# Kernel tuning notes

Measured on AMD Instinct MI355X. Metric: run time of the kernel, lower is better.

Reference implementation:

```python
import jax, jax.numpy as jnp
import numpy as np

N_NODES = 100000
N_EDGES = 1600000
IN_C, HID_C, OUT_C = 128, 64, 40


def setup_inputs() -> dict:
    key = jax.random.key(0)
    ks = jax.random.split(key, 8)
    x = jax.random.normal(ks[0], (N_NODES, IN_C), dtype=jnp.float32)
    edge_index = jax.random.randint(ks[1], (2, N_EDGES), 0, N_NODES, dtype=jnp.int64)
    # Glorot-ish init for weights
    W1 = jax.random.normal(ks[2], (IN_C, HID_C), dtype=jnp.float32) / np.sqrt(IN_C)
    W2 = jax.random.normal(ks[3], (HID_C, HID_C), dtype=jnp.float32) / np.sqrt(HID_C)
    W3 = jax.random.normal(ks[4], (HID_C, OUT_C), dtype=jnp.float32) / np.sqrt(HID_C)
    b1 = jnp.zeros((HID_C,), jnp.float32)
    b2 = jnp.zeros((HID_C,), jnp.float32)
    b3 = jnp.zeros((OUT_C,), jnp.float32)
    return {"x": x, "edge_index": edge_index, "W1": W1, "b1": b1,
            "W2": W2, "b2": b2, "W3": W3, "b3": b3}


def _gcn_prep(edge_index, num_nodes):
    # PyG GCNConv: add self-loops, symmetric normalization with edge_weight=1.
    src = jnp.concatenate([edge_index[0], jnp.arange(num_nodes, dtype=edge_index.dtype)])
    dst = jnp.concatenate([edge_index[1], jnp.arange(num_nodes, dtype=edge_index.dtype)])
    deg = jax.ops.segment_sum(jnp.ones_like(dst, dtype=jnp.float32), dst,
                              num_segments=num_nodes)
    dis = jnp.where(deg > 0, jax.lax.rsqrt(deg), 0.0)  # deg^-1/2, inf->0
    norm = dis[src] * dis[dst]  # per-edge symmetric norm
    return src, dst, norm


def _gcn_conv(x, W, b, src, dst, norm, num_nodes):
    h = x @ W                                # [N, F_out], linear (no bias)
    msg = h[src] * norm[:, None]             # gather + scale, [E_total, F_out]
    out = jax.ops.segment_sum(msg, dst, num_segments=num_nodes)
    return out + b                           # conv bias after aggregation


def reference(x, edge_index, W1, b1, W2, b2, W3, b3):
    n = x.shape[0]
    src, dst, norm = _gcn_prep(edge_index, n)
    h = jax.nn.relu(_gcn_conv(x, W1, b1, src, dst, norm, n))
    h = jax.nn.relu(_gcn_conv(h, W2, b2, src, dst, norm, n))
    h = _gcn_conv(h, W3, b3, src, dst, norm, n)
    return jax.nn.log_softmax(h, axis=1)
```

## Files before the change

### kernel.cpp

```cpp
#include <hip/hip_runtime.h>
#include <cstdint>
#include <cstddef>
#include <math.h>

#define NN 100000
#define NE 1600000
#define NB ((NN + 255) / 256)
#define EB 400
#define EPB (NE / EB)
#define CAP 5120

#define GT_NODES 128
#define GT_KC 32
#define GT_STRIDE 132

typedef unsigned short u16;

__device__ __forceinline__ float bf2f(u16 u) {
    union { unsigned i; float f; } c; c.i = ((unsigned)u) << 16; return c.f;
}
__device__ __forceinline__ u16 f2bf(float f) {
    union { float f; unsigned int i; } c; c.f = f;
    unsigned int lsb = (c.i >> 16) & 1u;
    return (u16)((c.i + 0x7fffu + lsb) >> 16);
}
__device__ __forceinline__ unsigned int pack2(float a, float b) {
    return (unsigned int)f2bf(a) | ((unsigned int)f2bf(b) << 16);
}

__device__ __forceinline__ int load_idx(const void* ei, int isI64, int pos) {
    if (isI64) return (int)((const long long*)ei)[pos];
    return ((const int*)ei)[pos];
}

__global__ __launch_bounds__(256) void k_build(const void* __restrict__ ei,
                                               int* __restrict__ cursor,
                                               int* __restrict__ csr_tmp) {
    __shared__ int sbuf[EPB];
    __shared__ int dbuf[EPB];
    __shared__ int cnt[NB];
    __shared__ int basel[NB];
    __shared__ int anynz;

    const int* p = (const int*)ei;
    if (threadIdx.x == 0) anynz = 0;
    for (int i = threadIdx.x; i < NB; i += 256) cnt[i] = 0;
    __syncthreads();
    int nz = 0;
    for (int i = threadIdx.x; i < 1024; i += 256) nz |= (p[2 * i + 1] != 0);
    if (nz) anynz = 1;
    __syncthreads();
    int isI64 = (anynz == 0);

    int base = blockIdx.x * EPB;
    for (int i = threadIdx.x; i < EPB; i += 256) {
        int s = load_idx(ei, isI64, base + i);
        int d = load_idx(ei, isI64, NE + base + i);
        sbuf[i] = s;
        dbuf[i] = d;
        atomicAdd(&cnt[d >> 8], 1);
    }
    __syncthreads();
    for (int j = threadIdx.x; j < NB; j += 256) {
        int c = cnt[j];
        int g = c ? atomicAdd(&cursor[j], c) : 0;
        basel[j] = j * CAP + g;
        cnt[j] = 0;
    }
    __syncthreads();
    for (int i = threadIdx.x; i < EPB; i += 256) {
        int s = sbuf[i];
        int d = dbuf[i];
        int bkt = d >> 8;
        int slot = basel[bkt] + atomicAdd(&cnt[bkt], 1);
        csr_tmp[slot] = ((d & 255) << 17) | s;
    }
}

__global__ __launch_bounds__(256) void k_sort(const int* __restrict__ cursor,
                                              const int* __restrict__ csr_tmp,
                                              int* __restrict__ csr,
                                              int* __restrict__ deg,
                                              int* __restrict__ offs,
                                              float* __restrict__ dis) {
    __shared__ int h[256];
    __shared__ int sc[256];
    __shared__ int cur[256];
    int j = blockIdx.x;
    int s0 = j * CAP, s1 = s0 + cursor[j];
    h[threadIdx.x] = 0;
    __syncthreads();
    for (int p = s0 + threadIdx.x; p < s1; p += 256)
        atomicAdd(&h[csr_tmp[p] >> 17], 1);
    __syncthreads();
    int v = h[threadIdx.x];
    sc[threadIdx.x] = v;
    __syncthreads();
#pragma unroll
    for (int off = 1; off < 256; off <<= 1) {
        int u = (threadIdx.x >= off) ? sc[threadIdx.x - off] : 0;
        __syncthreads();
        sc[threadIdx.x] += u;
        __syncthreads();
    }
    int excl = sc[threadIdx.x] - v;
    int node = j * 256 + threadIdx.x;
    if (node < NN) {
        deg[node] = v;
        offs[node] = s0 + excl;
        dis[node] = rsqrtf((float)(v + 1));
    }
    cur[threadIdx.x] = excl;
    __syncthreads();
    for (int p = s0 + threadIdx.x; p < s1; p += 256) {
        int pk = csr_tmp[p];
        int dl = pk >> 17;
        int pos = s0 + atomicAdd(&cur[dl], 1);
        csr[pos] = pk & 0x1FFFF;
    }
}

template <int K, int FR, bool RELU>
__global__ __launch_bounds__(512) void k_gemm(const float* __restrict__ x,
                                              const float* __restrict__ W,
                                              const float* __restrict__ dis,
                                              u16* __restrict__ out) {
    __shared__ float xT[GT_KC * GT_STRIDE];
    __shared__ float Wc[GT_KC * 64];
    const int tid = threadIdx.x;
    const int r = tid >> 4;
    const int c = tid & 15;
    const int f4 = tid & 7;
    const int nrow = tid >> 3;
    const int nbase = blockIdx.x * GT_NODES;

    float acc[4][4];
#pragma unroll
    for (int i = 0; i < 4; ++i)
#pragma unroll
        for (int j = 0; j < 4; ++j) acc[i][j] = 0.f;

    for (int kc = 0; kc < K; kc += GT_KC) {
#pragma unroll
        for (int q = 0; q < 4; ++q) {
            int e = q * 512 + tid;
            int kk = e >> 6, j = e & 63;
            Wc[kk * 64 + j] = (j < FR) ? W[(size_t)(kc + kk) * FR + j] : 0.f;
        }
#pragma unroll
        for (int q = 0; q < 2; ++q) {
            int nl = q * 64 + nrow;
            int n = nbase + nl;
            float4 v = make_float4(0.f, 0.f, 0.f, 0.f);
            if (n < NN) v = *(const float4*)(x + (size_t)n * K + kc + f4 * 4);
            if (RELU) {
                v.x = fmaxf(v.x, 0.f); v.y = fmaxf(v.y, 0.f);
                v.z = fmaxf(v.z, 0.f); v.w = fmaxf(v.w, 0.f);
            }
            xT[(f4 * 4 + 0) * GT_STRIDE + nl] = v.x;
            xT[(f4 * 4 + 1) * GT_STRIDE + nl] = v.y;
            xT[(f4 * 4 + 2) * GT_STRIDE + nl] = v.z;
            xT[(f4 * 4 + 3) * GT_STRIDE + nl] = v.w;
        }
        __syncthreads();
#pragma unroll 8
        for (int kk = 0; kk < GT_KC; ++kk) {
            float4 a = *(const float4*)&xT[kk * GT_STRIDE + r * 4];
            float4 w = *(const float4*)&Wc[kk * 64 + c * 4];
            float xa[4] = {a.x, a.y, a.z, a.w};
            float wb[4] = {w.x, w.y, w.z, w.w};
#pragma unroll
            for (int i = 0; i < 4; ++i)
#pragma unroll
                for (int j = 0; j < 4; ++j)
                    acc[i][j] = fmaf(xa[i], wb[j], acc[i][j]);
        }
        __syncthreads();
    }
    if (c * 4 < FR) {
#pragma unroll
        for (int i = 0; i < 4; ++i) {
            int n = nbase + r * 4 + i;
            if (n < NN) {
                float dv = dis[n];
                uint2 o;
                o.x = pack2(dv * acc[i][0], dv * acc[i][1]);
                o.y = pack2(dv * acc[i][2], dv * acc[i][3]);
                *(uint2*)(out + (size_t)n * FR + c * 4) = o;
            }
        }
    }
}

template <int F, int B, bool MASK>
__device__ __forceinline__ float gb(int myidx, int i, int lim,
                                    const u16* __restrict__ g, unsigned fc) {
    const u16* rp[B];
#pragma unroll
    for (int k = 0; k < B; ++k) {
        int s = __builtin_amdgcn_readlane(myidx, i + k);
        rp[k] = g + (size_t)(unsigned)s * (unsigned)F;
    }
    u16 hh[B];
#pragma unroll
    for (int k = 0; k < B; ++k) hh[k] = rp[k][fc];
    float t0 = 0.f, t1 = 0.f, t2 = 0.f, t3 = 0.f;
#pragma unroll
    for (int k = 0; k < B; ++k) {
        float v = bf2f(hh[k]);
        if (MASK) v = (i + k < lim) ? v : 0.f;
        if ((k & 3) == 0) t0 += v;
        else if ((k & 3) == 1) t1 += v;
        else if ((k & 3) == 2) t2 += v;
        else t3 += v;
    }
    return (t0 + t1) + (t2 + t3);
}

template <int F, bool SOFTMAX>
__global__ __launch_bounds__(256) void k_gather(const int* __restrict__ offs,
                                                const int* __restrict__ deg,
                                                const int* __restrict__ csr,
                                                const float* __restrict__ dis,
                                                const u16* __restrict__ g,
                                                const float* __restrict__ b,
                                                float* __restrict__ out) {
    int n = blockIdx.x * 4 + (threadIdx.x >> 6);
    unsigned f = threadIdx.x & 63;
    if (n >= NN) return;
    unsigned fc = (f < (unsigned)F) ? f : 0u;
    int start = __builtin_amdgcn_readfirstlane(offs[n]);
    int len   = __builtin_amdgcn_readfirstlane(deg[n]);
    float dvn = dis[n];
    float bf  = b[fc];
    float acc = bf2f(g[(unsigned)n * F + fc]);

    int myidx = 0;
    if ((int)f < len) myidx = csr[start + (int)f];
    int lim = (len < 64) ? len : 64;

    if (lim > 0) {
        if (lim >= 33) {
            int i = 0;
            for (; i + 16 <= lim; i += 16)
                acc += gb<F, 16, false>(myidx, i, lim, g, fc);
            if (i < lim)
                acc += gb<F, 16, true>(myidx, i, lim, g, fc);
        } else if (lim >= 17) {
            acc += gb<F, 32, true>(myidx, 0, lim, g, fc);
        } else if (lim == 16) {
            acc += gb<F, 16, false>(myidx, 0, lim, g, fc);
        } else {
            acc += gb<F, 16, true>(myidx, 0, lim, g, fc);
        }
    }

    if (len > 64) {
        int ii = 64;
        for (; ii + 2 <= len; ii += 2) {
            int s0 = __builtin_amdgcn_readfirstlane(csr[start + ii + 0]);
            int s1 = __builtin_amdgcn_readfirstlane(csr[start + ii + 1]);
            u16 h0 = g[(unsigned)s0 * F + fc];
            u16 h1 = g[(unsigned)s1 * F + fc];
            acc += bf2f(h0) + bf2f(h1);
        }
        if (ii < len) {
            int s0 = __builtin_amdgcn_readfirstlane(csr[start + ii]);
            acc += bf2f(g[(unsigned)s0 * F + fc]);
        }
    }

    float v = dvn * acc + bf;
    if (!SOFTMAX) {
        if (f < (unsigned)F) out[(size_t)n * F + f] = v;
    } else {
        float vv = (f < (unsigned)F) ? v : -INFINITY;
        float m = vv;
#pragma unroll
        for (int off = 32; off; off >>= 1) m = fmaxf(m, __shfl_xor(m, off));
        float ex = (f < (unsigned)F) ? __expf(vv - m) : 0.f;
        float sum = ex;
#pragma unroll
        for (int off = 32; off; off >>= 1) sum += __shfl_xor(sum, off);
        if (f < (unsigned)F) out[(size_t)n * F + f] = vv - m - logf(sum);
    }
}

extern "C" void kernel_launch(void* const* d_in, const int* in_sizes, int n_in,
                              void* d_out, int out_size, void* d_ws, size_t ws_size,
                              hipStream_t stream) {
    const float* x  = (const float*)d_in[0];
    const void*  ei = d_in[1];
    const float* W1 = (const float*)d_in[2];
    const float* b1 = (const float*)d_in[3];
    const float* W2 = (const float*)d_in[4];
    const float* b2 = (const float*)d_in[5];
    const float* W3 = (const float*)d_in[6];
    const float* b3 = (const float*)d_in[7];
    float* out = (float*)d_out;

    char* ws = (char*)d_ws;
    size_t off = 0;
    auto alloc = [&](size_t bytes) { void* p = ws + off; off += (bytes + 255) & ~255ULL; return p; };
    int*   cursor  = (int*)alloc(NB * 4);
    int*   deg     = (int*)alloc(NN * 4);
    float* dis     = (float*)alloc(NN * 4);
    int*   offs    = (int*)alloc(NN * 4);
    int*   csr_tmp = (int*)alloc((size_t)NB * CAP * 4);
    int*   csr     = (int*)alloc((size_t)NB * CAP * 4);
    u16*   gbuf    = (u16*)alloc((size_t)NN * 64 * 2);
    float* act     = (float*)alloc((size_t)NN * 64 * 4);

    hipMemsetAsync(cursor, 0, NB * 4, stream);
    k_build<<<EB, 256, 0, stream>>>(ei, cursor, csr_tmp);
    k_sort<<<NB, 256, 0, stream>>>(cursor, csr_tmp, csr, deg, offs, dis);

    const int gemm_grid = (NN + GT_NODES - 1) / GT_NODES;
    const int gather_grid = (NN + 3) / 4;

    k_gemm<128, 64, false><<<gemm_grid, 512, 0, stream>>>(x, W1, dis, gbuf);
    k_gather<64, false><<<gather_grid, 256, 0, stream>>>(offs, deg, csr, dis, gbuf, b1, act);

    k_gemm<64, 64, true><<<gemm_grid, 512, 0, stream>>>(act, W2, dis, gbuf);
    k_gather<64, false><<<gather_grid, 256, 0, stream>>>(offs, deg, csr, dis, gbuf, b2, act);

    k_gemm<64, 40, true><<<gemm_grid, 512, 0, stream>>>(act, W3, dis, gbuf);
    k_gather<40, true><<<gather_grid, 256, 0, stream>>>(offs, deg, csr, dis, gbuf, b3, out);
}
```

Before: 323.0 us.

## Gather two bf16 features per lane and split edges across half-waves

The gather kernel now has each lane load a packed pair of bf16 features as one 32-bit word. The two 32-lane halves of each wavefront process alternate edges and are combined with a cross-half shuffle. This halves the number of load instructions per edge row, widens loads and output stores, and shortens the softmax reductions. It adds a final cross-lane reduction and the __shfl-based index broadcast. The grid size drops the round-up and bounds check, which relies on NN being divisible by 4.

```diff
diff --git a/kernel.cpp b/kernel.cpp
--- a/kernel.cpp
+++ b/kernel.cpp
@@ -193,96 +193,119 @@
 }
 
 template <int F, int B, bool MASK>
-__device__ __forceinline__ float gb(int myidx, int i, int lim,
-                                    const u16* __restrict__ g, unsigned fc) {
-    const u16* rp[B];
-#pragma unroll
-    for (int k = 0; k < B; ++k) {
-        int s = __builtin_amdgcn_readlane(myidx, i + k);
-        rp[k] = g + (size_t)(unsigned)s * (unsigned)F;
-    }
-    u16 hh[B];
-#pragma unroll
-    for (int k = 0; k < B; ++k) hh[k] = rp[k][fc];
-    float t0 = 0.f, t1 = 0.f, t2 = 0.f, t3 = 0.f;
-#pragma unroll
-    for (int k = 0; k < B; ++k) {
-        float v = bf2f(hh[k]);
-        if (MASK) v = (i + k < lim) ? v : 0.f;
-        if ((k & 3) == 0) t0 += v;
-        else if ((k & 3) == 1) t1 += v;
-        else if ((k & 3) == 2) t2 += v;
-        else t3 += v;
-    }
-    return (t0 + t1) + (t2 + t3);
+__device__ __forceinline__ float2 gb2(int myidx, int i, int lim, int eh,
+                                      const u16* __restrict__ g, unsigned fp) {
+    unsigned off[B / 2];
+#pragma unroll
+    for (int k = 0; k < B / 2; ++k) {
+        int s = __shfl(myidx, i + 2 * k + eh);
+        off[k] = (unsigned)s * (unsigned)(F * 2) + fp * 4u;
+    }
+    unsigned hv[B / 2];
+#pragma unroll
+    for (int k = 0; k < B / 2; ++k)
+        hv[k] = *(const unsigned*)((const char*)g + off[k]);
+    float x0 = 0.f, x1 = 0.f, y0 = 0.f, y1 = 0.f;
+#pragma unroll
+    for (int k = 0; k < B / 2; ++k) {
+        float vx = bf2f((u16)(hv[k] & 0xffffu));
+        float vy = bf2f((u16)(hv[k] >> 16));
+        if (MASK) {
+            bool ok = (i + 2 * k + eh) < lim;
+            vx = ok ? vx : 0.f;
+            vy = ok ? vy : 0.f;
+        }
+        if (k & 1) { x1 += vx; y1 += vy; }
+        else       { x0 += vx; y0 += vy; }
+    }
+    float2 r; r.x = x0 + x1; r.y = y0 + y1; return r;
 }
 
 template <int F, bool SOFTMAX>
-__global__ __launch_bounds__(256) void k_gather(const int* __restrict__ offs,
-                                                const int* __restrict__ deg,
-                                                const int* __restrict__ csr,
-                                                const float* __restrict__ dis,
-                                                const u16* __restrict__ g,
-                                                const float* __restrict__ b,
-                                                float* __restrict__ out) {
+__global__ __launch_bounds__(256) void k_gather2(const int* __restrict__ offs,
+                                                 const int* __restrict__ deg,
+                                                 const int* __restrict__ csr,
+                                                 const float* __restrict__ dis,
+                                                 const u16* __restrict__ g,
+                                                 const float* __restrict__ b,
+                                                 float* __restrict__ out) {
     int n = blockIdx.x * 4 + (threadIdx.x >> 6);
-    unsigned f = threadIdx.x & 63;
-    if (n >= NN) return;
-    unsigned fc = (f < (unsigned)F) ? f : 0u;
+    unsigned lane = threadIdx.x & 63;
+    unsigned fc2 = lane & 31;
+    int eh = (int)(lane >> 5);
+    bool valid = (2u * fc2 < (unsigned)F);
+    unsigned fp = valid ? fc2 : (unsigned)(F / 2 - 1);
+
     int start = __builtin_amdgcn_readfirstlane(offs[n]);
     int len   = __builtin_amdgcn_readfirstlane(deg[n]);
     float dvn = dis[n];
-    float bf  = b[fc];
-    float acc = bf2f(g[(unsigned)n * F + fc]);
+
+    unsigned sv = *(const unsigned*)((const char*)g
+                      + (size_t)(unsigned)n * (unsigned)(F * 2) + fp * 4u);
+    float2 acc;
+    acc.x = eh ? 0.f : bf2f((u16)(sv & 0xffffu));
+    acc.y = eh ? 0.f : bf2f((u16)(sv >> 16));
 
     int myidx = 0;
-    if ((int)f < len) myidx = csr[start + (int)f];
+    if ((int)lane < len) myidx = csr[start + (int)lane];
     int lim = (len < 64) ? len : 64;
 
     if (lim > 0) {
+        float2 t;
         if (lim >= 33) {
             int i = 0;
-            for (; i + 16 <= lim; i += 16)
-                acc += gb<F, 16, false>(myidx, i, lim, g, fc);
-            if (i < lim)
-                acc += gb<F, 16, true>(myidx, i, lim, g, fc);
+            for (; i + 16 <= lim; i += 16) {
+                t = gb2<F, 16, false>(myidx, i, lim, eh, g, fp);
+                acc.x += t.x; acc.y += t.y;
+            }
+            if (i < lim) {
+                t = gb2<F, 16, true>(myidx, i, lim, eh, g, fp);
+                acc.x += t.x; acc.y += t.y;
+            }
         } else if (lim >= 17) {
-            acc += gb<F, 32, true>(myidx, 0, lim, g, fc);
+            t = gb2<F, 32, true>(myidx, 0, lim, eh, g, fp);
+            acc.x += t.x; acc.y += t.y;
         } else if (lim == 16) {
-            acc += gb<F, 16, false>(myidx, 0, lim, g, fc);
+            t = gb2<F, 16, false>(myidx, 0, lim, eh, g, fp);
+            acc.x += t.x; acc.y += t.y;
         } else {
-            acc += gb<F, 16, true>(myidx, 0, lim, g, fc);
-        }
-    }
-
+            t = gb2<F, 16, true>(myidx, 0, lim, eh, g, fp);
+            acc.x += t.x; acc.y += t.y;
+        }
+    }
     if (len > 64) {
-        int ii = 64;
-        for (; ii + 2 <= len; ii += 2) {
-            int s0 = __builtin_amdgcn_readfirstlane(csr[start + ii + 0]);
-            int s1 = __builtin_amdgcn_readfirstlane(csr[start + ii + 1]);
-            u16 h0 = g[(unsigned)s0 * F + fc];
-            u16 h1 = g[(unsigned)s1 * F + fc];
-            acc += bf2f(h0) + bf2f(h1);
-        }
-        if (ii < len) {
-            int s0 = __builtin_amdgcn_readfirstlane(csr[start + ii]);
-            acc += bf2f(g[(unsigned)s0 * F + fc]);
-        }
-    }
-
-    float v = dvn * acc + bf;
+        for (int i = 64 + eh; i < len; i += 2) {
+            int s = csr[start + i];
+            unsigned hv = *(const unsigned*)((const char*)g
+                              + (unsigned)s * (unsigned)(F * 2) + fp * 4u);
+            acc.x += bf2f((u16)(hv & 0xffffu));
+            acc.y += bf2f((u16)(hv >> 16));
+        }
+    }
+    acc.x += __shfl_xor(acc.x, 32);
+    acc.y += __shfl_xor(acc.y, 32);
+
+    float vx = dvn * acc.x + b[2 * fp + 0];
+    float vy = dvn * acc.y + b[2 * fp + 1];
+
     if (!SOFTMAX) {
-        if (f < (unsigned)F) out[(size_t)n * F + f] = v;
+        if (eh == 0 && valid) {
+            float2 o; o.x = vx; o.y = vy;
+            *(float2*)(out + (size_t)n * F + 2 * fp) = o;
+        }
     } else {
-        float vv = (f < (unsigned)F) ? v : -INFINITY;
-        float m = vv;
-#pragma unroll
-        for (int off = 32; off; off >>= 1) m = fmaxf(m, __shfl_xor(m, off));
-        float ex = (f < (unsigned)F) ? __expf(vv - m) : 0.f;
+        float m = valid ? fmaxf(vx, vy) : -INFINITY;
+#pragma unroll
+        for (int off = 16; off; off >>= 1) m = fmaxf(m, __shfl_xor(m, off));
+        float ex = valid ? (__expf(vx - m) + __expf(vy - m)) : 0.f;
         float sum = ex;
 #pragma unroll
-        for (int off = 32; off; off >>= 1) sum += __shfl_xor(sum, off);
-        if (f < (unsigned)F) out[(size_t)n * F + f] = vv - m - logf(sum);
+        for (int off = 16; off; off >>= 1) sum += __shfl_xor(sum, off);
+        if (eh == 0 && valid) {
+            float ls = logf(sum);
+            float2 o; o.x = vx - m - ls; o.y = vy - m - ls;
+            *(float2*)(out + (size_t)n * F + 2 * fp) = o;
+        }
     }
 }
 
@@ -316,14 +339,14 @@
     k_sort<<<NB, 256, 0, stream>>>(cursor, csr_tmp, csr, deg, offs, dis);
 
     const int gemm_grid = (NN + GT_NODES - 1) / GT_NODES;
-    const int gather_grid = (NN + 3) / 4;
+    const int gather_grid = NN / 4;
 
     k_gemm<128, 64, false><<<gemm_grid, 512, 0, stream>>>(x, W1, dis, gbuf);
-    k_gather<64, false><<<gather_grid, 256, 0, stream>>>(offs, deg, csr, dis, gbuf, b1, act);
+    k_gather2<64, false><<<gather_grid, 256, 0, stream>>>(offs, deg, csr, dis, gbuf, b1, act);
 
     k_gemm<64, 64, true><<<gemm_grid, 512, 0, stream>>>(act, W2, dis, gbuf);
-    k_gather<64, false><<<gather_grid, 256, 0, stream>>>(offs, deg, csr, dis, gbuf, b2, act);
+    k_gather2<64, false><<<gather_grid, 256, 0, stream>>>(offs, deg, csr, dis, gbuf, b2, act);
 
     k_gemm<64, 40, true><<<gemm_grid, 512, 0, stream>>>(act, W3, dis, gbuf);
-    k_gather<40, true><<<gather_grid, 256, 0, stream>>>(offs, deg, csr, dis, gbuf, b3, out);
-}
+    k_gather2<40, true><<<gather_grid, 256, 0, stream>>>(offs, deg, csr, dis, gbuf, b3, out);
+}
```

New measurement: 328.3 us. Within noise of the previous version (+1.6%).
